# Kernel optimization log

Hardware: AMD Instinct MI355X
Metric: run time of the kernel (lower is better)

The kernel has to match this reference:

```python
import jax, jax.numpy as jnp
import numpy as np

B, N, D = 32, 128, 64
E = N * N
EPS = 1e-5


def _bn(x, gamma, beta):
    # torch BatchNorm1d on (B, C, D): normalize per-channel over (batch, last dim)
    mean = jnp.mean(x, axis=(0, 2), keepdims=True)
    var = jnp.var(x, axis=(0, 2), keepdims=True)
    return (x - mean) * jax.lax.rsqrt(var + EPS) * gamma[None, :, None] + beta[None, :, None]


def _gat_layer(x, edge, Wh, We, Wp, Wa, gv, bv, ge, be):
    b, n, d = x.shape
    res = x
    z_h = jnp.einsum('bnd,od->bno', x, Wh)   # fc_h (torch Linear: y = x W^T)
    z_e = jnp.einsum('bed,od->beo', edge, We)  # fc_e
    # incidence matmuls are pure gathers: edge e = i*n + j
    z_src = jnp.broadcast_to(z_h[:, None, :, :], (b, n, n, d)).reshape(b, n * n, d)  # start: edge (i,j) <- node j
    z_dst = jnp.broadcast_to(z_h[:, :, None, :], (b, n, n, d)).reshape(b, n * n, d)  # end:   edge (i,j) <- node i
    z = jnp.concatenate([z_src, z_dst, z_e], axis=-1)  # (b, E, 3d)
    z_e_new = jnp.einsum('bec,oc->beo', z, Wp)  # fc_proj
    attn = jnp.einsum('bec,c->be', z, Wa[0])    # attn_fc -> (b, E)
    attn = jnp.where(attn >= 0, attn, 0.01 * attn)  # LeakyReLU(0.01)
    attn = jax.nn.softmax(attn.reshape(b, n, n), axis=2).reshape(b, n * n)  # softmax over sources j
    # scatter via end^T: node i <- sum_j attn[i,j] * z_src[i*n+j]
    agg = (attn[:, :, None] * z_src).reshape(b, n, n, d).sum(axis=2)
    x_new = jax.nn.elu(res + _bn(agg, gv, bv))
    edge_new = jax.nn.elu(_bn(z_e_new, ge, be))
    return x_new, edge_new


def setup_inputs():
    key = jax.random.key(0)
    ks = jax.random.split(key, 10)
    scale = float(np.sqrt(2.0 / D))
    return {
        'x': jax.random.normal(ks[0], (B, N, D), jnp.float32),
        'edge': jax.random.normal(ks[1], (B, E, D), jnp.float32),
        'Wh1': jax.random.normal(ks[2], (D, D), jnp.float32) * scale,
        'We1': jax.random.normal(ks[3], (D, D), jnp.float32) * scale,
        'Wp1': jax.random.normal(ks[4], (D, 3 * D), jnp.float32) * scale,
        'Wa1': jax.random.normal(ks[5], (1, 3 * D), jnp.float32) * scale,
        'Wh2': jax.random.normal(ks[6], (D, D), jnp.float32) * scale,
        'We2': jax.random.normal(ks[7], (D, D), jnp.float32) * scale,
        'Wp2': jax.random.normal(ks[8], (D, 3 * D), jnp.float32) * scale,
        'Wa2': jax.random.normal(ks[9], (1, 3 * D), jnp.float32) * scale,
        'gv1': jnp.ones((N,), jnp.float32), 'bv1': jnp.zeros((N,), jnp.float32),
        'ge1': jnp.ones((E,), jnp.float32), 'be1': jnp.zeros((E,), jnp.float32),
        'gv2': jnp.ones((N,), jnp.float32), 'bv2': jnp.zeros((N,), jnp.float32),
        'ge2': jnp.ones((E,), jnp.float32), 'be2': jnp.zeros((E,), jnp.float32),
    }


def reference(x, edge, Wh1, We1, Wp1, Wa1, Wh2, We2, Wp2, Wa2,
              gv1, bv1, ge1, be1, gv2, bv2, ge2, be2):
    x, edge = _gat_layer(x, edge, Wh1, We1, Wp1, Wa1, gv1, bv1, ge1, be1)
    x, edge = _gat_layer(x, edge, Wh2, We2, Wp2, Wa2, gv2, bv2, ge2, be2)
    return x, edge
```

## Files before the change

kernel.cpp:

```cpp
#include <hip/hip_runtime.h>
#include <math.h>

#define BB 32
#define NN 128
#define DD 64
#define EE (NN*NN)
#define EPSI 1e-5f

typedef __attribute__((ext_vector_type(8))) short bf16x8;
typedef __attribute__((ext_vector_type(4))) float f32x4;
typedef __attribute__((ext_vector_type(4))) short s16x4;

__device__ __forceinline__ short f2bf(float f) {
    union { float f; unsigned u; } v; v.f = f;
    unsigned u = v.u;
    unsigned r = (u + 0x7FFFu + ((u >> 16) & 1u)) >> 16;
    return (short)r;
}
__device__ __forceinline__ float elu(float v) {
    return v > 0.f ? v : __expf(v) - 1.f;
}

__global__ void k_fold(const float* __restrict__ Wp, const float* __restrict__ We,
                       const float* __restrict__ Wa,
                       short* __restrict__ Mbf, short* __restrict__ wbf)
{
    int t = blockIdx.x * 256 + threadIdx.x;
    int d = t >> 6, k = t & 63;
    float acc = 0.f;
    for (int o = 0; o < DD; ++o)
        acc += Wp[d*192 + 128 + o] * We[o*DD + k];
    Mbf[d*DD + k] = f2bf(acc);
    if (d == 0) {
        float aw = 0.f;
        for (int o = 0; o < DD; ++o)
            aw += Wa[128 + o] * We[o*DD + k];
        wbf[k] = f2bf(aw);
    }
}

__global__ void k_node(const float* __restrict__ x, const float* __restrict__ Wh,
                       const float* __restrict__ Wp, const float* __restrict__ Wa,
                       float* __restrict__ zh, float* __restrict__ Ps,
                       float* __restrict__ Pd, float* __restrict__ sO,
                       float* __restrict__ tO)
{
    int row = blockIdx.x;
    int d = threadIdx.x;
    __shared__ float xr[DD];
    __shared__ float zr[DD];
    xr[d] = x[row*DD + d];
    __syncthreads();
    float acc = 0.f;
#pragma unroll
    for (int k = 0; k < DD; ++k) acc += xr[k] * Wh[d*DD + k];
    zr[d] = acc;
    zh[row*DD + d] = acc;
    __syncthreads();
    float a0 = 0.f, a1 = 0.f;
#pragma unroll
    for (int o = 0; o < DD; ++o) {
        float z = zr[o];
        a0 += Wp[d*192 + o]      * z;
        a1 += Wp[d*192 + 64 + o] * z;
    }
    Ps[row*DD + d] = a0;
    Pd[row*DD + d] = a1;
    float sv = zr[d] * Wa[d];
    float tv = zr[d] * Wa[64 + d];
#pragma unroll
    for (int off = 32; off; off >>= 1) {
        sv += __shfl_xor(sv, off);
        tv += __shfl_xor(tv, off);
    }
    if (d == 0) { sO[row] = sv; tO[row] = tv; }
}

template <int INM, int OUTM>
__global__ __launch_bounds__(256, 4) void k_edge(
    const void* __restrict__ einv,
    const short* __restrict__ Mbf,
    const short* __restrict__ wbf,
    const float* __restrict__ Ps,
    const float* __restrict__ Pd,
    const float* __restrict__ ge, const float* __restrict__ be,
    void* __restrict__ eoutv, float* __restrict__ uout)
{
    __shared__ float zl[4][32][68];
    const int l  = threadIdx.x & 63;
    const int wv = threadIdx.x >> 6;
    const int lr = l & 15;
    const int lg = l >> 4;
    const int e  = blockIdx.x * 4 + wv;
    const int i0 = e >> 7, j0 = e & 127;
    float (*Z)[68] = zl[wv];

    bf16x8 afr[2][2];
    if constexpr (INM == 0) {
        const float* ein = (const float*)einv;
#pragma unroll
        for (int m = 0; m < 2; ++m) {
            const float* rowp = ein + ((size_t)(16*m + lr)*EE + e)*DD;
            const float4 v0 = *reinterpret_cast<const float4*>(rowp +      lg*8);
            const float4 v1 = *reinterpret_cast<const float4*>(rowp +      lg*8 + 4);
            const float4 v2 = *reinterpret_cast<const float4*>(rowp + 32 + lg*8);
            const float4 v3 = *reinterpret_cast<const float4*>(rowp + 32 + lg*8 + 4);
            afr[m][0][0]=f2bf(v0.x); afr[m][0][1]=f2bf(v0.y); afr[m][0][2]=f2bf(v0.z); afr[m][0][3]=f2bf(v0.w);
            afr[m][0][4]=f2bf(v1.x); afr[m][0][5]=f2bf(v1.y); afr[m][0][6]=f2bf(v1.z); afr[m][0][7]=f2bf(v1.w);
            afr[m][1][0]=f2bf(v2.x); afr[m][1][1]=f2bf(v2.y); afr[m][1][2]=f2bf(v2.z); afr[m][1][3]=f2bf(v2.w);
            afr[m][1][4]=f2bf(v3.x); afr[m][1][5]=f2bf(v3.y); afr[m][1][6]=f2bf(v3.z); afr[m][1][7]=f2bf(v3.w);
        }
    } else {
        const short* ein = (const short*)einv + (size_t)e*BB*DD;
#pragma unroll
        for (int m = 0; m < 2; ++m)
#pragma unroll
            for (int s = 0; s < 2; ++s)
                afr[m][s] = *reinterpret_cast<const bf16x8*>(ein + (16*m + lr)*DD + s*32 + lg*8);
    }

    bf16x8 bfr[4][2];
#pragma unroll
    for (int n = 0; n < 4; ++n)
#pragma unroll
        for (int s = 0; s < 2; ++s)
            bfr[n][s] = *reinterpret_cast<const bf16x8*>(Mbf + (16*n + lr)*DD + s*32 + lg*8);
    const bf16x8 zerov = (bf16x8){0,0,0,0,0,0,0,0};
    bf16x8 wfrag[2];
#pragma unroll
    for (int s = 0; s < 2; ++s)
        wfrag[s] = (lr == 0) ? *reinterpret_cast<const bf16x8*>(wbf + s*32 + lg*8) : zerov;

    f32x4 acc[2][4];
    f32x4 uacc[2];
#pragma unroll
    for (int m = 0; m < 2; ++m) {
        uacc[m] = (f32x4){0.f, 0.f, 0.f, 0.f};
#pragma unroll
        for (int n = 0; n < 4; ++n)
            acc[m][n] = (f32x4){0.f, 0.f, 0.f, 0.f};
    }
#pragma unroll
    for (int m = 0; m < 2; ++m) {
#pragma unroll
        for (int n = 0; n < 4; ++n)
            acc[m][n] = __builtin_amdgcn_mfma_f32_16x16x32_bf16(afr[m][0], bfr[n][0], acc[m][n], 0, 0, 0);
        uacc[m] = __builtin_amdgcn_mfma_f32_16x16x32_bf16(afr[m][0], wfrag[0], uacc[m], 0, 0, 0);
#pragma unroll
        for (int n = 0; n < 4; ++n)
            acc[m][n] = __builtin_amdgcn_mfma_f32_16x16x32_bf16(afr[m][1], bfr[n][1], acc[m][n], 0, 0, 0);
        uacc[m] = __builtin_amdgcn_mfma_f32_16x16x32_bf16(afr[m][1], wfrag[1], uacc[m], 0, 0, 0);
    }

#pragma unroll
    for (int m = 0; m < 2; ++m)
#pragma unroll
        for (int n = 0; n < 4; ++n)
#pragma unroll
            for (int q = 0; q < 4; ++q)
                Z[16*m + 4*lg + q][16*n + lr] = acc[m][n][q];

    float s1 = 0.f, s2 = 0.f;
#pragma unroll
    for (int it = 0; it < 8; ++it) {
        const int b = lg + 4*it;
        float4 z = *reinterpret_cast<float4*>(&Z[b][lr*4]);
        const float4 ps = *reinterpret_cast<const float4*>(Ps + ((size_t)(b*NN + j0))*DD + lr*4);
        const float4 pd = *reinterpret_cast<const float4*>(Pd + ((size_t)(b*NN + i0))*DD + lr*4);
        z.x += ps.x + pd.x; z.y += ps.y + pd.y;
        z.z += ps.z + pd.z; z.w += ps.w + pd.w;
        s1 += z.x + z.y + z.z + z.w;
        s2 += z.x*z.x + z.y*z.y + z.z*z.z + z.w*z.w;
        *reinterpret_cast<float4*>(&Z[b][lr*4]) = z;
    }
#pragma unroll
    for (int off = 1; off < 64; off <<= 1) {
        s1 += __shfl_xor(s1, off);
        s2 += __shfl_xor(s2, off);
    }
    const float mean = s1 * (1.f/2048.f);
    const float var  = s2 * (1.f/2048.f) - mean*mean;
    const float sc = ge[e] * rsqrtf(var + EPSI);
    const float sh = be[e] - mean*sc;

    if constexpr (OUTM == 0) {
        float* eout = (float*)eoutv;
#pragma unroll
        for (int it = 0; it < 8; ++it) {
            const int b = lg + 4*it;
            float4 z = *reinterpret_cast<float4*>(&Z[b][lr*4]);
            z.x = elu(z.x*sc + sh);
            z.y = elu(z.y*sc + sh);
            z.z = elu(z.z*sc + sh);
            z.w = elu(z.w*sc + sh);
            *reinterpret_cast<float4*>(eout + ((size_t)b*EE + e)*DD + lr*4) = z;
        }
    } else {
        short* eout = (short*)eoutv + (size_t)e*BB*DD;
#pragma unroll
        for (int it = 0; it < 8; ++it) {
            const int b = 4*it + lg;
            const int c0 = lr*4;
            float4 z = *reinterpret_cast<float4*>(&Z[b][c0]);
            s16x4 o;
            o[0] = f2bf(elu(z.x*sc + sh));
            o[1] = f2bf(elu(z.y*sc + sh));
            o[2] = f2bf(elu(z.z*sc + sh));
            o[3] = f2bf(elu(z.w*sc + sh));
            *reinterpret_cast<s16x4*>(eout + b*DD + c0) = o;
        }
    }

    if (lr == 0) {
#pragma unroll
        for (int m = 0; m < 2; ++m)
#pragma unroll
            for (int q = 0; q < 4; ++q)
                uout[(size_t)(16*m + 4*lg + q)*EE + e] = uacc[m][q];
    }
}

__global__ void k_attn(const float* __restrict__ sI, const float* __restrict__ tI,
                       const float* __restrict__ u, const float* __restrict__ zh,
                       float* __restrict__ agg)
{
    int blk = blockIdx.x; int b = blk >> 7, i = blk & 127;
    int l = threadIdx.x;
    __shared__ float at[NN];
    float ti = tI[blk];
    float l0 = sI[b*NN + l]      + ti + u[b*EE + i*NN + l];
    float l1 = sI[b*NN + l + 64] + ti + u[b*EE + i*NN + l + 64];
    l0 = l0 >= 0.f ? l0 : 0.01f*l0;
    l1 = l1 >= 0.f ? l1 : 0.01f*l1;
    float mx = fmaxf(l0, l1);
#pragma unroll
    for (int off = 32; off; off >>= 1) mx = fmaxf(mx, __shfl_xor(mx, off));
    float e0 = __expf(l0 - mx), e1 = __expf(l1 - mx);
    float sm = e0 + e1;
#pragma unroll
    for (int off = 32; off; off >>= 1) sm += __shfl_xor(sm, off);
    float inv = 1.f / sm;
    at[l]      = e0 * inv;
    at[l + 64] = e1 * inv;
    __syncthreads();
    float acc = 0.f;
    for (int j = 0; j < NN; ++j) acc += at[j] * zh[(b*NN + j)*DD + l];
    agg[(b*NN + i)*DD + l] = acc;
}

__global__ void k_vbn(const float* __restrict__ agg, const float* __restrict__ xres,
                      const float* __restrict__ gv, const float* __restrict__ bv,
                      float* __restrict__ xout)
{
    int i = blockIdx.x, t = threadIdx.x;
    float vals[8];
    float s1 = 0.f, s2 = 0.f;
#pragma unroll
    for (int q = 0; q < 8; ++q) {
        int m = t + 256*q; int b = m >> 6, d = m & 63;
        float v = agg[(b*NN + i)*DD + d];
        vals[q] = v; s1 += v; s2 += v*v;
    }
#pragma unroll
    for (int off = 1; off < 64; off <<= 1) {
        s1 += __shfl_xor(s1, off);
        s2 += __shfl_xor(s2, off);
    }
    __shared__ float r1[4], r2[4];
    int wv = t >> 6;
    if ((t & 63) == 0) { r1[wv] = s1; r2[wv] = s2; }
    __syncthreads();
    s1 = r1[0] + r1[1] + r1[2] + r1[3];
    s2 = r2[0] + r2[1] + r2[2] + r2[3];
    float mean  = s1 * (1.f/2048.f);
    float var   = s2 * (1.f/2048.f) - mean*mean;
    float scale = gv[i] * rsqrtf(var + EPSI);
    float shift = bv[i] - mean*scale;
#pragma unroll
    for (int q = 0; q < 8; ++q) {
        int m = t + 256*q; int b = m >> 6, d = m & 63;
        float v = vals[q]*scale + shift + xres[(b*NN + i)*DD + d];
        xout[(b*NN + i)*DD + d] = v > 0.f ? v : __expf(v) - 1.f;
    }
}

extern "C" void kernel_launch(void* const* d_in, const int* in_sizes, int n_in,
                              void* d_out, int out_size, void* d_ws, size_t ws_size,
                              hipStream_t stream)
{
    const float* x    = (const float*)d_in[0];
    const float* edge = (const float*)d_in[1];
    const float* Wh1  = (const float*)d_in[2];
    const float* We1  = (const float*)d_in[3];
    const float* Wp1  = (const float*)d_in[4];
    const float* Wa1  = (const float*)d_in[5];
    const float* Wh2  = (const float*)d_in[6];
    const float* We2  = (const float*)d_in[7];
    const float* Wp2  = (const float*)d_in[8];
    const float* Wa2  = (const float*)d_in[9];
    const float* gv1  = (const float*)d_in[10];
    const float* bv1  = (const float*)d_in[11];
    const float* ge1  = (const float*)d_in[12];
    const float* be1  = (const float*)d_in[13];
    const float* gv2  = (const float*)d_in[14];
    const float* bv2  = (const float*)d_in[15];
    const float* ge2  = (const float*)d_in[16];
    const float* be2  = (const float*)d_in[17];

    float* xout = (float*)d_out;
    float* eout = (float*)d_out + BB*NN*DD;

    float* ws  = (float*)d_ws;
    short* Mbf = (short*)ws;  ws += DD*DD/2;
    short* wbf = (short*)ws;  ws += DD/2;
    float* zh  = ws;  ws += BB*NN*DD;
    float* Ps  = ws;  ws += BB*NN*DD;
    float* Pd  = ws;  ws += BB*NN*DD;
    float* sb  = ws;  ws += BB*NN;
    float* tb  = ws;  ws += BB*NN;
    float* ub  = ws;  ws += BB*EE;
    float* agg = ws;  ws += BB*NN*DD;
    float* x1  = ws;  ws += BB*NN*DD;
    short* e1bf = (short*)ws;
    const size_t need = ((size_t)(ws - (float*)d_ws))*4 + (size_t)EE*BB*DD*2;

    const bool dense = (ws_size >= need);

    k_fold<<<16, 256, 0, stream>>>(Wp1, We1, Wa1, Mbf, wbf);
    k_node<<<BB*NN, 64, 0, stream>>>(x, Wh1, Wp1, Wa1, zh, Ps, Pd, sb, tb);
    if (dense)
        k_edge<0,1><<<EE/4, 256, 0, stream>>>(edge, Mbf, wbf, Ps, Pd, ge1, be1, e1bf, ub);
    else
        k_edge<0,0><<<EE/4, 256, 0, stream>>>(edge, Mbf, wbf, Ps, Pd, ge1, be1, eout, ub);
    k_attn<<<BB*NN, 64, 0, stream>>>(sb, tb, ub, zh, agg);
    k_vbn<<<NN, 256, 0, stream>>>(agg, x, gv1, bv1, x1);
    k_fold<<<16, 256, 0, stream>>>(Wp2, We2, Wa2, Mbf, wbf);
    k_node<<<BB*NN, 64, 0, stream>>>(x1, Wh2, Wp2, Wa2, zh, Ps, Pd, sb, tb);
    if (dense)
        k_edge<1,0><<<EE/4, 256, 0, stream>>>(e1bf, Mbf, wbf, Ps, Pd, ge2, be2, eout, ub);
    else
        k_edge<0,0><<<EE/4, 256, 0, stream>>>(eout, Mbf, wbf, Ps, Pd, ge2, be2, eout, ub);
    k_attn<<<BB*NN, 64, 0, stream>>>(sb, tb, ub, zh, agg);
    k_vbn<<<NN, 256, 0, stream>>>(agg, x1, gv2, bv2, xout);
}
```

Baseline: 214.7 us.

## Store node projections in MFMA fragment layout and keep edge BN in registers

k_node now writes Ps/Pd transposed into a per-node layout matching the MFMA accumulator fragment order. k_edge can then initialise its accumulators directly from coalesced float4 loads instead of doing strided per-batch loads after an LDS round trip. BatchNorm statistics and the ELU are computed in registers. LDS is used only to transpose for the output stores, in two halves, which halves the shared-memory footprint. The bf16 output is now written with 16-byte vectors, at the cost of extra waitcnt barriers and a more intricate index mapping.

```diff
diff --git a/kernel.cpp b/kernel.cpp
--- a/kernel.cpp
+++ b/kernel.cpp
@@ -9,7 +9,6 @@
 
 typedef __attribute__((ext_vector_type(8))) short bf16x8;
 typedef __attribute__((ext_vector_type(4))) float f32x4;
-typedef __attribute__((ext_vector_type(4))) short s16x4;
 
 __device__ __forceinline__ short f2bf(float f) {
     union { float f; unsigned u; } v; v.f = f;
@@ -41,11 +40,12 @@
 
 __global__ void k_node(const float* __restrict__ x, const float* __restrict__ Wh,
                        const float* __restrict__ Wp, const float* __restrict__ Wa,
-                       float* __restrict__ zh, float* __restrict__ Ps,
-                       float* __restrict__ Pd, float* __restrict__ sO,
+                       float* __restrict__ zh, float* __restrict__ PsT,
+                       float* __restrict__ PdT, float* __restrict__ sO,
                        float* __restrict__ tO)
 {
     int row = blockIdx.x;
+    int b = row >> 7, n = row & 127;
     int d = threadIdx.x;
     __shared__ float xr[DD];
     __shared__ float zr[DD];
@@ -64,8 +64,9 @@
         a0 += Wp[d*192 + o]      * z;
         a1 += Wp[d*192 + 64 + o] * z;
     }
-    Ps[row*DD + d] = a0;
-    Pd[row*DD + d] = a1;
+    const int fi = ((b >> 4)*4 + (d >> 4))*256 + (((b >> 2) & 3)*16 + (d & 15))*4 + (b & 3);
+    PsT[n*2048 + fi] = a0;
+    PdT[n*2048 + fi] = a1;
     float sv = zr[d] * Wa[d];
     float tv = zr[d] * Wa[64 + d];
 #pragma unroll
@@ -81,12 +82,12 @@
     const void* __restrict__ einv,
     const short* __restrict__ Mbf,
     const short* __restrict__ wbf,
-    const float* __restrict__ Ps,
-    const float* __restrict__ Pd,
+    const float* __restrict__ PsT,
+    const float* __restrict__ PdT,
     const float* __restrict__ ge, const float* __restrict__ be,
     void* __restrict__ eoutv, float* __restrict__ uout)
 {
-    __shared__ float zl[4][32][68];
+    __shared__ float zl[4][16][68];
     const int l  = threadIdx.x & 63;
     const int wv = threadIdx.x >> 6;
     const int lr = l & 15;
@@ -133,13 +134,21 @@
 
     f32x4 acc[2][4];
     f32x4 uacc[2];
-#pragma unroll
-    for (int m = 0; m < 2; ++m) {
-        uacc[m] = (f32x4){0.f, 0.f, 0.f, 0.f};
-#pragma unroll
-        for (int n = 0; n < 4; ++n)
-            acc[m][n] = (f32x4){0.f, 0.f, 0.f, 0.f};
-    }
+    {
+        const float* psb = PsT + j0*2048;
+        const float* pdb = PdT + i0*2048;
+#pragma unroll
+        for (int m = 0; m < 2; ++m) {
+            uacc[m] = (f32x4){0.f, 0.f, 0.f, 0.f};
+#pragma unroll
+            for (int n = 0; n < 4; ++n) {
+                const float4 a = *reinterpret_cast<const float4*>(psb + (m*4+n)*256 + l*4);
+                const float4 c = *reinterpret_cast<const float4*>(pdb + (m*4+n)*256 + l*4);
+                acc[m][n] = (f32x4){a.x+c.x, a.y+c.y, a.z+c.z, a.w+c.w};
+            }
+        }
+    }
+
 #pragma unroll
     for (int m = 0; m < 2; ++m) {
 #pragma unroll
@@ -152,27 +161,13 @@
         uacc[m] = __builtin_amdgcn_mfma_f32_16x16x32_bf16(afr[m][1], wfrag[1], uacc[m], 0, 0, 0);
     }
 
+    float s1 = 0.f, s2 = 0.f;
 #pragma unroll
     for (int m = 0; m < 2; ++m)
 #pragma unroll
         for (int n = 0; n < 4; ++n)
 #pragma unroll
-            for (int q = 0; q < 4; ++q)
-                Z[16*m + 4*lg + q][16*n + lr] = acc[m][n][q];
-
-    float s1 = 0.f, s2 = 0.f;
-#pragma unroll
-    for (int it = 0; it < 8; ++it) {
-        const int b = lg + 4*it;
-        float4 z = *reinterpret_cast<float4*>(&Z[b][lr*4]);
-        const float4 ps = *reinterpret_cast<const float4*>(Ps + ((size_t)(b*NN + j0))*DD + lr*4);
-        const float4 pd = *reinterpret_cast<const float4*>(Pd + ((size_t)(b*NN + i0))*DD + lr*4);
-        z.x += ps.x + pd.x; z.y += ps.y + pd.y;
-        z.z += ps.z + pd.z; z.w += ps.w + pd.w;
-        s1 += z.x + z.y + z.z + z.w;
-        s2 += z.x*z.x + z.y*z.y + z.z*z.z + z.w*z.w;
-        *reinterpret_cast<float4*>(&Z[b][lr*4]) = z;
-    }
+            for (int q = 0; q < 4; ++q) { float v = acc[m][n][q]; s1 += v; s2 += v*v; }
 #pragma unroll
     for (int off = 1; off < 64; off <<= 1) {
         s1 += __shfl_xor(s1, off);
@@ -183,33 +178,13 @@
     const float sc = ge[e] * rsqrtf(var + EPSI);
     const float sh = be[e] - mean*sc;
 
-    if constexpr (OUTM == 0) {
-        float* eout = (float*)eoutv;
-#pragma unroll
-        for (int it = 0; it < 8; ++it) {
-            const int b = lg + 4*it;
-            float4 z = *reinterpret_cast<float4*>(&Z[b][lr*4]);
-            z.x = elu(z.x*sc + sh);
-            z.y = elu(z.y*sc + sh);
-            z.z = elu(z.z*sc + sh);
-            z.w = elu(z.w*sc + sh);
-            *reinterpret_cast<float4*>(eout + ((size_t)b*EE + e)*DD + lr*4) = z;
-        }
-    } else {
-        short* eout = (short*)eoutv + (size_t)e*BB*DD;
-#pragma unroll
-        for (int it = 0; it < 8; ++it) {
-            const int b = 4*it + lg;
-            const int c0 = lr*4;
-            float4 z = *reinterpret_cast<float4*>(&Z[b][c0]);
-            s16x4 o;
-            o[0] = f2bf(elu(z.x*sc + sh));
-            o[1] = f2bf(elu(z.y*sc + sh));
-            o[2] = f2bf(elu(z.z*sc + sh));
-            o[3] = f2bf(elu(z.w*sc + sh));
-            *reinterpret_cast<s16x4*>(eout + b*DD + c0) = o;
-        }
-    }
+#pragma unroll
+    for (int m = 0; m < 2; ++m)
+#pragma unroll
+        for (int n = 0; n < 4; ++n)
+#pragma unroll
+            for (int q = 0; q < 4; ++q)
+                acc[m][n][q] = elu(acc[m][n][q]*sc + sh);
 
     if (lr == 0) {
 #pragma unroll
@@ -217,6 +192,41 @@
 #pragma unroll
             for (int q = 0; q < 4; ++q)
                 uout[(size_t)(16*m + 4*lg + q)*EE + e] = uacc[m][q];
+    }
+
+#pragma unroll
+    for (int h = 0; h < 2; ++h) {
+#pragma unroll
+        for (int n = 0; n < 4; ++n)
+#pragma unroll
+            for (int q = 0; q < 4; ++q)
+                Z[4*lg + q][16*n + lr] = acc[h][n][q];
+        __builtin_amdgcn_s_waitcnt(0);
+        if constexpr (OUTM == 0) {
+            float* eout = (float*)eoutv;
+#pragma unroll
+            for (int it = 0; it < 4; ++it) {
+                const int rr = lg + 4*it;
+                const int b  = 16*h + rr;
+                float4 z = *reinterpret_cast<float4*>(&Z[rr][lr*4]);
+                *reinterpret_cast<float4*>(eout + ((size_t)b*EE + e)*DD + lr*4) = z;
+            }
+        } else {
+            short* eout = (short*)eoutv + (size_t)e*BB*DD;
+#pragma unroll
+            for (int it = 0; it < 2; ++it) {
+                const int rr = (l >> 3) + 8*it;
+                const int b  = 16*h + rr;
+                const int c0 = (l & 7)*8;
+                float4 zlo = *reinterpret_cast<float4*>(&Z[rr][c0]);
+                float4 zhi = *reinterpret_cast<float4*>(&Z[rr][c0+4]);
+                bf16x8 o;
+                o[0]=f2bf(zlo.x); o[1]=f2bf(zlo.y); o[2]=f2bf(zlo.z); o[3]=f2bf(zlo.w);
+                o[4]=f2bf(zhi.x); o[5]=f2bf(zhi.y); o[6]=f2bf(zhi.z); o[7]=f2bf(zhi.w);
+                *reinterpret_cast<bf16x8*>(eout + b*DD + c0) = o;
+            }
+        }
+        __builtin_amdgcn_s_waitcnt(0);
     }
 }
 
@@ -314,8 +324,8 @@
     short* Mbf = (short*)ws;  ws += DD*DD/2;
     short* wbf = (short*)ws;  ws += DD/2;
     float* zh  = ws;  ws += BB*NN*DD;
-    float* Ps  = ws;  ws += BB*NN*DD;
-    float* Pd  = ws;  ws += BB*NN*DD;
+    float* PsT = ws;  ws += NN*BB*DD;
+    float* PdT = ws;  ws += NN*BB*DD;
     float* sb  = ws;  ws += BB*NN;
     float* tb  = ws;  ws += BB*NN;
     float* ub  = ws;  ws += BB*EE;
@@ -327,19 +337,19 @@
     const bool dense = (ws_size >= need);
 
     k_fold<<<16, 256, 0, stream>>>(Wp1, We1, Wa1, Mbf, wbf);
-    k_node<<<BB*NN, 64, 0, stream>>>(x, Wh1, Wp1, Wa1, zh, Ps, Pd, sb, tb);
+    k_node<<<BB*NN, 64, 0, stream>>>(x, Wh1, Wp1, Wa1, zh, PsT, PdT, sb, tb);
     if (dense)
-        k_edge<0,1><<<EE/4, 256, 0, stream>>>(edge, Mbf, wbf, Ps, Pd, ge1, be1, e1bf, ub);
+        k_edge<0,1><<<EE/4, 256, 0, stream>>>(edge, Mbf, wbf, PsT, PdT, ge1, be1, e1bf, ub);
     else
-        k_edge<0,0><<<EE/4, 256, 0, stream>>>(edge, Mbf, wbf, Ps, Pd, ge1, be1, eout, ub);
+        k_edge<0,0><<<EE/4, 256, 0, stream>>>(edge, Mbf, wbf, PsT, PdT, ge1, be1, eout, ub);
     k_attn<<<BB*NN, 64, 0, stream>>>(sb, tb, ub, zh, agg);
     k_vbn<<<NN, 256, 0, stream>>>(agg, x, gv1, bv1, x1);
     k_fold<<<16, 256, 0, stream>>>(Wp2, We2, Wa2, Mbf, wbf);
-    k_node<<<BB*NN, 64, 0, stream>>>(x1, Wh2, Wp2, Wa2, zh, Ps, Pd, sb, tb);
+    k_node<<<BB*NN, 64, 0, stream>>>(x1, Wh2, Wp2, Wa2, zh, PsT, PdT, sb, tb);
     if (dense)
-        k_edge<1,0><<<EE/4, 256, 0, stream>>>(e1bf, Mbf, wbf, Ps, Pd, ge2, be2, eout, ub);
+        k_edge<1,0><<<EE/4, 256, 0, stream>>>(e1bf, Mbf, wbf, PsT, PdT, ge2, be2, eout, ub);
     else
-        k_edge<0,0><<<EE/4, 256, 0, stream>>>(eout, Mbf, wbf, Ps, Pd, ge2, be2, eout, ub);
+        k_edge<0,0><<<EE/4, 256, 0, stream>>>(eout, Mbf, wbf, PsT, PdT, ge2, be2, eout, ub);
     k_attn<<<BB*NN, 64, 0, stream>>>(sb, tb, ub, zh, agg);
     k_vbn<<<NN, 256, 0, stream>>>(agg, x1, gv2, bv2, xout);
 }
```

Measured after the change: 217.3 us. Within noise of the previous version (+1.2%).
